# Kernel optimization log

Measured on AMD Instinct MI355X. Metric: run time of the kernel, lower is better.

## Reference

```python
import jax, jax.numpy as jnp
import numpy as np
from jax import lax

B, D, HID, H = 4096, 2048, 2048, 8
HS = HID // H            # head size (also input block size since D == HID)
P = int(HID * 4 / 3)     # 2730 up-projection dim
EPS = 1e-5


def setup_inputs() -> dict:
    key = jax.random.key(0)
    ks = iter(jax.random.split(key, 48))
    def nrm(shape, s=0.02):
        return jax.random.normal(next(ks), shape, jnp.float32) * s
    inp = {
        "x": jax.random.normal(next(ks), (B, D), jnp.float32),
        "h_prev": jax.random.normal(next(ks), (B, HID), jnp.float32),
        "c_prev": jax.random.normal(next(ks), (B, HID), jnp.float32),
        "n_prev": jnp.ones((B, HID), jnp.float32),
        "m_prev": jnp.zeros((B, HID), jnp.float32),
        "ln_w": jnp.ones((D,), jnp.float32),
        "ln_b": jnp.zeros((D,), jnp.float32),
        "conv_w": nrm((1, 1, 4), 0.3),  # Conv1d(1,1,4) kernel
        "conv_b": jnp.zeros((1,), jnp.float32),
        "gn_w": jnp.ones((HID,), jnp.float32),
        "gn_b": jnp.zeros((HID,), jnp.float32),
        "upL_w": nrm((HID, P)), "upL_b": jnp.zeros((P,), jnp.float32),
        "upR_w": nrm((HID, P)), "upR_b": jnp.zeros((P,), jnp.float32),
        "down_w": nrm((P, D)), "down_b": jnp.zeros((D,), jnp.float32),
    }
    # 8 block-diagonal projections: weight [H, block_in, block_out], bias [H, block_out]
    for name in ["Wz", "Wi", "Wf", "Wo", "Rz", "Ri", "Rf", "Ro"]:
        inp[name + "_w"] = nrm((H, HS, HS), 0.05)
        inp[name + "_b"] = jnp.zeros((H, HS), jnp.float32)
    return inp


def _bd(v, w, b):
    # block-diagonal linear: v [B, H*bi], w [H, bi, bo], b [H, bo] -> [B, H*bo]
    Bv = v.shape[0]
    Hn, bi, bo = w.shape
    y = jnp.einsum('bhi,hio->bho', v.reshape(Bv, Hn, bi), w) + b
    return y.reshape(Bv, Hn * bo)


def _forward(x, h_prev, c_prev, n_prev, m_prev, ln_w, ln_b, conv_w, conv_b,
             Wz_w, Wz_b, Wi_w, Wi_b, Wf_w, Wf_b, Wo_w, Wo_b,
             Rz_w, Rz_b, Ri_w, Ri_b, Rf_w, Rf_b, Ro_w, Ro_b,
             gn_w, gn_b, upL_w, upL_b, upR_w, upR_b, down_w, down_b):
    # LayerNorm over features
    mu = x.mean(-1, keepdims=True)
    var = ((x - mu) ** 2).mean(-1, keepdims=True)
    x_norm = (x - mu) * lax.rsqrt(var + EPS) * ln_w + ln_b
    # causal conv1d (kernel 4): left-pad 3, same as padding=3 then crop right 3
    xc = lax.conv_general_dilated(x_norm[:, None, :], conv_w, (1,), [(3, 0)],
                                  dimension_numbers=('NCH', 'OIH', 'NCH'))
    x_conv = jax.nn.silu(xc[:, 0, :] + conv_b)
    # gates via block-diagonal projections
    z = jnp.tanh(_bd(x, Wz_w, Wz_b) + _bd(h_prev, Rz_w, Rz_b))
    o = jax.nn.sigmoid(_bd(x, Wo_w, Wo_b) + _bd(h_prev, Ro_w, Ro_b))
    i_tilde = _bd(x_conv, Wi_w, Wi_b) + _bd(h_prev, Ri_w, Ri_b)
    f_tilde = _bd(x_conv, Wf_w, Wf_b) + _bd(h_prev, Rf_w, Rf_b)
    # stabilized exponential gating
    m_t = jnp.maximum(f_tilde + m_prev, i_tilde)
    i_g = jnp.exp(i_tilde - m_t)
    f_g = jnp.exp(f_tilde + m_prev - m_t)
    c_t = f_g * c_prev + i_g * z
    n_t = f_g * n_prev + i_g
    h_t = o * c_t / n_t
    # GroupNorm(num_heads groups) over hidden
    g = h_t.reshape(-1, H, HS)
    gm = g.mean(-1, keepdims=True)
    gv = ((g - gm) ** 2).mean(-1, keepdims=True)
    gn = ((g - gm) * lax.rsqrt(gv + EPS)).reshape(-1, HID) * gn_w + gn_b
    # gated MLP up/down projection + residual
    left = gn @ upL_w + upL_b
    right = gn @ upR_w + upR_b
    out = (left * jax.nn.gelu(right, approximate=False)) @ down_w + down_b + x
    return out, h_t, c_t, n_t, m_t


def reference(x, h_prev, c_prev, n_prev, m_prev, ln_w, ln_b, conv_w, conv_b,
              Wz_w, Wz_b, Wi_w, Wi_b, Wf_w, Wf_b, Wo_w, Wo_b,
              Rz_w, Rz_b, Ri_w, Ri_b, Rf_w, Rf_b, Ro_w, Ro_b,
              gn_w, gn_b, upL_w, upL_b, upR_w, upR_b, down_w, down_b):
    return _forward(x, h_prev, c_prev, n_prev, m_prev, ln_w, ln_b, conv_w, conv_b,
                    Wz_w, Wz_b, Wi_w, Wi_b, Wf_w, Wf_b, Wo_w, Wo_b,
                    Rz_w, Rz_b, Ri_w, Ri_b, Rf_w, Rf_b, Ro_w, Ro_b,
                    gn_w, gn_b, upL_w, upL_b, upR_w, upR_b, down_w, down_b)
```

## Files before the change

kernel.cpp:

```cpp
#include <hip/hip_runtime.h>
#include <stdint.h>
#include <math.h>

#define Bn   4096
#define Dn   2048
#define Hn   8
#define HSn  256
#define Pn   2730
#define PPADn 2816
#define EPSn 1e-5f

using f32x4  = __attribute__((ext_vector_type(4))) float;
using bf16x8 = __attribute__((ext_vector_type(8))) short;
using u16x4  = __attribute__((ext_vector_type(4))) unsigned short;

__device__ __forceinline__ unsigned short f2bf(float f) {
  union { float f; uint32_t u; } x; x.f = f;
  uint32_t u = x.u;
  return (unsigned short)((u + 0x7FFFu + ((u >> 16) & 1u)) >> 16);
}

__device__ __forceinline__ int xcd_swz(int bid, int n) {
  return (bid & 7) * (n >> 3) + (bid >> 3);
}

#define GLDS(gp, lp) __builtin_amdgcn_global_load_lds(                        \
    (__attribute__((address_space(1))) void*)(size_t)(gp),                    \
    (__attribute__((address_space(3))) void*)(lp), 16, 0, 0)

__device__ __forceinline__ void gemm_mainloop(
    const ushort* __restrict__ A, int lda,
    const ushort* __restrict__ Bt, int ldb,
    int K, int row0, int col0,
    ushort* Asm, ushort* Bsm, f32x4 acc[4][4])
{
  const int tid  = threadIdx.x;
  const int wid  = tid >> 6;
  const int lane = tid & 63;
  const int l16  = lane & 15, lhi = lane >> 4;
  const int wm   = (wid >> 1) * 64, wn = (wid & 1) * 64;
  const int nk   = K >> 6;

  for (int kt = 0; kt < nk; ++kt) {
    __syncthreads();
    #pragma unroll
    for (int q = 0; q < 4; ++q) {
      int ee = q * 256 + tid;
      int r = ee >> 3, c = (ee & 7) << 3;
      const ushort* ga = A  + (size_t)(row0 + r) * lda + (size_t)kt * 64 + c;
      GLDS(ga, (char*)Asm + (q * 4096 + wid * 1024));
      const ushort* gb = Bt + (size_t)(col0 + r) * ldb + (size_t)kt * 64 + c;
      GLDS(gb, (char*)Bsm + (q * 4096 + wid * 1024));
    }
    __syncthreads();
    #pragma unroll
    for (int kk = 0; kk < 2; ++kk) {
      bf16x8 af[4], bfr[4];
      #pragma unroll
      for (int i = 0; i < 4; ++i) {
        af[i]  = *(const bf16x8*)(Asm + (wm + i * 16 + l16) * 64 + kk * 32 + lhi * 8);
        bfr[i] = *(const bf16x8*)(Bsm + (wn + i * 16 + l16) * 64 + kk * 32 + lhi * 8);
      }
      #pragma unroll
      for (int i = 0; i < 4; ++i)
        #pragma unroll
        for (int j = 0; j < 4; ++j)
          acc[i][j] = __builtin_amdgcn_mfma_f32_16x16x32_bf16(af[i], bfr[j], acc[i][j], 0, 0, 0);
    }
  }
}

__global__ void transpose_cvt_kernel(const float* __restrict__ in, ushort* __restrict__ out,
                                     int R, int C, int Rpad, int Cpad)
{
  __shared__ float tile[32][33];
  int r0 = blockIdx.y * 32, c0 = blockIdx.x * 32;
  int tx = threadIdx.x, ty = threadIdx.y;
  #pragma unroll
  for (int i = 0; i < 32; i += 8) {
    int r = r0 + ty + i, c = c0 + tx;
    tile[ty + i][tx] = (r < R && c < C) ? in[(size_t)r * C + c] : 0.f;
  }
  __syncthreads();
  #pragma unroll
  for (int i = 0; i < 32; i += 8) {
    int cc = c0 + ty + i, rr = r0 + tx;
    if (cc < Cpad && rr < Rpad)
      out[(size_t)cc * Rpad + rr] = f2bf(tile[tx][ty + i]);
  }
}

struct Ptr8 { const float* p[8]; };

__global__ void gate_wcvt_kernel(Ptr8 src, ushort* __restrict__ out)
{
  __shared__ float tile[32][33];
  int tz = blockIdx.z;
  int tensor = tz >> 3, h = tz & 7;
  const float* in = src.p[tensor] + (size_t)h * HSn * HSn;
  ushort* o = out + (size_t)tz * HSn * HSn;
  int r0 = blockIdx.y * 32, c0 = blockIdx.x * 32;
  int tx = threadIdx.x, ty = threadIdx.y;
  #pragma unroll
  for (int i = 0; i < 32; i += 8)
    tile[ty + i][tx] = in[(size_t)(r0 + ty + i) * HSn + c0 + tx];
  __syncthreads();
  #pragma unroll
  for (int i = 0; i < 32; i += 8)
    o[(size_t)(c0 + ty + i) * HSn + (r0 + tx)] = f2bf(tile[tx][ty + i]);
}

__global__ void cvt_bf16_kernel(const float* __restrict__ in, ushort* __restrict__ out, int n8)
{
  int idx = blockIdx.x * blockDim.x + threadIdx.x;
  if (idx >= n8) return;
  float4 a = ((const float4*)in)[idx * 2];
  float4 b = ((const float4*)in)[idx * 2 + 1];
  bf16x8 v;
  v[0] = (short)f2bf(a.x); v[1] = (short)f2bf(a.y);
  v[2] = (short)f2bf(a.z); v[3] = (short)f2bf(a.w);
  v[4] = (short)f2bf(b.x); v[5] = (short)f2bf(b.y);
  v[6] = (short)f2bf(b.z); v[7] = (short)f2bf(b.w);
  ((bf16x8*)out)[idx] = v;
}

__global__ __launch_bounds__(256) void ln_conv_kernel(
    const float* __restrict__ x, const float* __restrict__ lnw, const float* __restrict__ lnb,
    const float* __restrict__ convw, const float* __restrict__ convb,
    ushort* __restrict__ xbf, ushort* __restrict__ xcbf)
{
  __shared__ float xn[Dn];
  __shared__ float red[8];
  const int b = blockIdx.x, t = threadIdx.x;
  const float* xr = x + (size_t)b * Dn;
  float4 v0 = ((const float4*)xr)[t * 2];
  float4 v1 = ((const float4*)xr)[t * 2 + 1];
  float xv[8] = {v0.x, v0.y, v0.z, v0.w, v1.x, v1.y, v1.z, v1.w};
  float s = 0.f, s2 = 0.f;
  #pragma unroll
  for (int e = 0; e < 8; ++e) { s += xv[e]; s2 += xv[e] * xv[e]; }
  #pragma unroll
  for (int off = 32; off >= 1; off >>= 1) {
    s  += __shfl_xor(s, off, 64);
    s2 += __shfl_xor(s2, off, 64);
  }
  int wid = t >> 6;
  if ((t & 63) == 0) { red[wid] = s; red[4 + wid] = s2; }
  __syncthreads();
  s  = red[0] + red[1] + red[2] + red[3];
  s2 = red[4] + red[5] + red[6] + red[7];
  float mean = s * (1.f / Dn);
  float var  = s2 * (1.f / Dn) - mean * mean;
  float rstd = rsqrtf(var + EPSn);

  float4 w0 = ((const float4*)lnw)[t * 2], w1 = ((const float4*)lnw)[t * 2 + 1];
  float4 b0 = ((const float4*)lnb)[t * 2], b1 = ((const float4*)lnb)[t * 2 + 1];
  float lw[8] = {w0.x, w0.y, w0.z, w0.w, w1.x, w1.y, w1.z, w1.w};
  float lb[8] = {b0.x, b0.y, b0.z, b0.w, b1.x, b1.y, b1.z, b1.w};
  bf16x8 xb;
  #pragma unroll
  for (int e = 0; e < 8; ++e) {
    int j = t * 8 + e;
    float nv = (xv[e] - mean) * rstd * lw[e] + lb[e];
    xn[j] = nv;
    xb[e] = (short)f2bf(xv[e]);
  }
  ((bf16x8*)(xbf + (size_t)b * Dn))[t] = xb;
  __syncthreads();
  float w[4] = {convw[0], convw[1], convw[2], convw[3]};
  float cb = convb[0];
  bf16x8 cv;
  #pragma unroll
  for (int e = 0; e < 8; ++e) {
    int j = t * 8 + e;
    float a0 = (j >= 3) ? xn[j - 3] : 0.f;
    float a1 = (j >= 2) ? xn[j - 2] : 0.f;
    float a2 = (j >= 1) ? xn[j - 1] : 0.f;
    float v = w[0] * a0 + w[1] * a1 + w[2] * a2 + w[3] * xn[j] + cb;
    float sv = v / (1.f + expf(-v));
    cv[e] = (short)f2bf(sv);
  }
  ((bf16x8*)(xcbf + (size_t)b * Dn))[t] = cv;
}

struct GateArgs { const float* wb[4]; const float* rb[4]; };

__global__ __launch_bounds__(256) void gate_gemm_kernel(
    const ushort* __restrict__ xbf, const ushort* __restrict__ xcbf,
    const ushort* __restrict__ hbf, const ushort* __restrict__ gWt,
    GateArgs gb, float* __restrict__ preact)
{
  __shared__ ushort Asm[128 * 64];
  __shared__ ushort Bsm[128 * 64];
  const int g = blockIdx.z, h = blockIdx.y;
  const int bx = xcd_swz(blockIdx.x, 64);
  const int mt = bx >> 1, nt = bx & 1;
  const int row0 = mt * 128, col0 = nt * 128;
  f32x4 acc[4][4];
  #pragma unroll
  for (int i = 0; i < 4; ++i)
    #pragma unroll
    for (int j = 0; j < 4; ++j) acc[i][j] = f32x4{0.f, 0.f, 0.f, 0.f};

  const ushort* A1 = ((g == 1 || g == 2) ? xcbf : xbf) + h * HSn;
  const ushort* B1 = gWt + (size_t)(g * 8 + h) * (HSn * HSn);
  gemm_mainloop(A1, Dn, B1, HSn, HSn, row0, col0, Asm, Bsm, acc);
  const ushort* A2 = hbf + h * HSn;
  const ushort* B2 = gWt + (size_t)((4 + g) * 8 + h) * (HSn * HSn);
  gemm_mainloop(A2, Dn, B2, HSn, HSn, row0, col0, Asm, Bsm, acc);

  const int tid = threadIdx.x, wid = tid >> 6, lane = tid & 63;
  const int l16 = lane & 15, lhi = lane >> 4;
  const int wm = (wid >> 1) * 64, wn = (wid & 1) * 64;
  float* out = preact + (size_t)g * ((size_t)Bn * Dn);
  const float* wb = gb.wb[g] + h * HSn;
  const float* rb = gb.rb[g] + h * HSn;
  #pragma unroll
  for (int j = 0; j < 4; ++j) {
    int cg = col0 + wn + j * 16 + l16;
    float bias = wb[cg] + rb[cg];
    #pragma unroll
    for (int i = 0; i < 4; ++i) {
      #pragma unroll
      for (int r = 0; r < 4; ++r) {
        int rg = row0 + wm + i * 16 + lhi * 4 + r;
        float v = acc[i][j][r] + bias;
        if (g == 0) v = tanhf(v);
        else if (g == 3) v = 1.f / (1.f + expf(-v));
        out[(size_t)rg * Dn + h * HSn + cg] = v;
      }
    }
  }
}

__global__ __launch_bounds__(64) void gate_pw_gn_kernel(
    const float* __restrict__ preact,
    const float* __restrict__ c_prev, const float* __restrict__ n_prev,
    const float* __restrict__ m_prev,
    const float* __restrict__ gn_w, const float* __restrict__ gn_b,
    float* __restrict__ o_h, float* __restrict__ o_c,
    float* __restrict__ o_n, float* __restrict__ o_m,
    ushort* __restrict__ gnbf)
{
  const int bh = blockIdx.x;
  const int b = bh >> 3, h = bh & 7;
  const int t = threadIdx.x;
  const size_t NE = (size_t)Bn * Dn;
  const size_t base = (size_t)b * Dn + h * HSn + t * 4;

  float4 z4 = *(const float4*)(preact + base);
  float4 i4 = *(const float4*)(preact + NE + base);
  float4 f4 = *(const float4*)(preact + 2 * NE + base);
  float4 o4 = *(const float4*)(preact + 3 * NE + base);
  float4 c4 = *(const float4*)(c_prev + base);
  float4 n4 = *(const float4*)(n_prev + base);
  float4 m4 = *(const float4*)(m_prev + base);

  float za[4] = {z4.x, z4.y, z4.z, z4.w};
  float ia[4] = {i4.x, i4.y, i4.z, i4.w};
  float fa[4] = {f4.x, f4.y, f4.z, f4.w};
  float oa[4] = {o4.x, o4.y, o4.z, o4.w};
  float ca[4] = {c4.x, c4.y, c4.z, c4.w};
  float na[4] = {n4.x, n4.y, n4.z, n4.w};
  float ma[4] = {m4.x, m4.y, m4.z, m4.w};

  float hv[4], mo[4], co[4], no[4];
  float s = 0.f, s2 = 0.f;
  #pragma unroll
  for (int e = 0; e < 4; ++e) {
    float mt = fmaxf(fa[e] + ma[e], ia[e]);
    float ig = expf(ia[e] - mt);
    float fg = expf(fa[e] + ma[e] - mt);
    float ct = fg * ca[e] + ig * za[e];
    float nt = fg * na[e] + ig;
    float ht = oa[e] * ct / nt;
    mo[e] = mt; co[e] = ct; no[e] = nt; hv[e] = ht;
    s += ht; s2 += ht * ht;
  }
  *(float4*)(o_m + base) = make_float4(mo[0], mo[1], mo[2], mo[3]);
  *(float4*)(o_c + base) = make_float4(co[0], co[1], co[2], co[3]);
  *(float4*)(o_n + base) = make_float4(no[0], no[1], no[2], no[3]);
  *(float4*)(o_h + base) = make_float4(hv[0], hv[1], hv[2], hv[3]);

  #pragma unroll
  for (int off = 32; off >= 1; off >>= 1) {
    s  += __shfl_xor(s, off, 64);
    s2 += __shfl_xor(s2, off, 64);
  }
  float mean = s * (1.f / HSn);
  float var  = s2 * (1.f / HSn) - mean * mean;
  float rstd = rsqrtf(var + EPSn);
  u16x4 gv;
  #pragma unroll
  for (int e = 0; e < 4; ++e) {
    int hid = h * HSn + t * 4 + e;
    float gval = (hv[e] - mean) * rstd * gn_w[hid] + gn_b[hid];
    gv[e] = f2bf(gval);
  }
  *(u16x4*)(gnbf + base) = gv;
}

__global__ __launch_bounds__(256) void up_gemm_kernel(
    const ushort* __restrict__ gnbf, const ushort* __restrict__ upt,
    const float* __restrict__ upb, float* __restrict__ leftbuf,
    ushort* __restrict__ actbf, int mode)
{
  __shared__ ushort Asm[128 * 64];
  __shared__ ushort Bsm[128 * 64];
  const int NT = PPADn / 128;
  const int bx = xcd_swz(blockIdx.x, 32 * NT);
  const int mt = bx / NT, nt = bx % NT;
  const int row0 = mt * 128, col0 = nt * 128;
  f32x4 acc[4][4];
  #pragma unroll
  for (int i = 0; i < 4; ++i)
    #pragma unroll
    for (int j = 0; j < 4; ++j) acc[i][j] = f32x4{0.f, 0.f, 0.f, 0.f};

  gemm_mainloop(gnbf, Dn, upt, Dn, Dn, row0, col0, Asm, Bsm, acc);

  const int tid = threadIdx.x, wid = tid >> 6, lane = tid & 63;
  const int l16 = lane & 15, lhi = lane >> 4;
  const int wm = (wid >> 1) * 64, wn = (wid & 1) * 64;
  #pragma unroll
  for (int j = 0; j < 4; ++j) {
    int col = col0 + wn + j * 16 + l16;
    float bias = (col < Pn) ? upb[col] : 0.f;
    #pragma unroll
    for (int i = 0; i < 4; ++i) {
      #pragma unroll
      for (int r = 0; r < 4; ++r) {
        int rg = row0 + wm + i * 16 + lhi * 4 + r;
        float v = acc[i][j][r] + bias;
        size_t idx = (size_t)rg * PPADn + col;
        if (mode == 0) {
          leftbuf[idx] = v;
        } else {
          float ge = 0.5f * v * (1.f + erff(v * 0.70710678118f));
          actbf[idx] = f2bf(leftbuf[idx] * ge);
        }
      }
    }
  }
}

__global__ __launch_bounds__(256) void down_gemm_kernel(
    const ushort* __restrict__ actbf, const ushort* __restrict__ downt,
    const float* __restrict__ downb, const float* __restrict__ x,
    float* __restrict__ outp)
{
  __shared__ ushort Asm[128 * 64];
  __shared__ ushort Bsm[128 * 64];
  const int NT = Dn / 128;
  const int bx = xcd_swz(blockIdx.x, 32 * NT);
  const int mt = bx / NT, nt = bx % NT;
  const int row0 = mt * 128, col0 = nt * 128;
  f32x4 acc[4][4];
  #pragma unroll
  for (int i = 0; i < 4; ++i)
    #pragma unroll
    for (int j = 0; j < 4; ++j) acc[i][j] = f32x4{0.f, 0.f, 0.f, 0.f};

  gemm_mainloop(actbf, PPADn, downt, PPADn, PPADn, row0, col0, Asm, Bsm, acc);

  const int tid = threadIdx.x, wid = tid >> 6, lane = tid & 63;
  const int l16 = lane & 15, lhi = lane >> 4;
  const int wm = (wid >> 1) * 64, wn = (wid & 1) * 64;
  #pragma unroll
  for (int j = 0; j < 4; ++j) {
    int col = col0 + wn + j * 16 + l16;
    float bias = downb[col];
    #pragma unroll
    for (int i = 0; i < 4; ++i) {
      #pragma unroll
      for (int r = 0; r < 4; ++r) {
        int rg = row0 + wm + i * 16 + lhi * 4 + r;
        size_t idx = (size_t)rg * Dn + col;
        outp[idx] = acc[i][j][r] + bias + x[idx];
      }
    }
  }
}

extern "C" void kernel_launch(void* const* d_in, const int* in_sizes, int n_in,
                              void* d_out, int out_size, void* d_ws, size_t ws_size,
                              hipStream_t stream)
{
  const float* x      = (const float*)d_in[0];
  const float* h_prev = (const float*)d_in[1];
  const float* c_prev = (const float*)d_in[2];
  const float* n_prev = (const float*)d_in[3];
  const float* m_prev = (const float*)d_in[4];
  const float* ln_w   = (const float*)d_in[5];
  const float* ln_b   = (const float*)d_in[6];
  const float* conv_w = (const float*)d_in[7];
  const float* conv_b = (const float*)d_in[8];
  const float* gn_w   = (const float*)d_in[9];
  const float* gn_b   = (const float*)d_in[10];
  const float* upL_w  = (const float*)d_in[11];
  const float* upL_b  = (const float*)d_in[12];
  const float* upR_w  = (const float*)d_in[13];
  const float* upR_b  = (const float*)d_in[14];
  const float* down_w = (const float*)d_in[15];
  const float* down_b = (const float*)d_in[16];

  const size_t NE = (size_t)Bn * Dn;

  char* ws = (char*)d_ws;
  size_t off = 0;
  auto alloc = [&](size_t bytes) { void* p = ws + off; off += (bytes + 255) & ~(size_t)255; return p; };
  ushort* xbf   = (ushort*)alloc(NE * 2);
  ushort* xcbf  = (ushort*)alloc(NE * 2);
  ushort* hbf   = (ushort*)alloc(NE * 2);
  ushort* gnbf  = (ushort*)alloc(NE * 2);
  ushort* gWt   = (ushort*)alloc((size_t)8 * Hn * HSn * HSn * 2);
  ushort* upLt  = (ushort*)alloc((size_t)PPADn * Dn * 2);
  ushort* upRt  = (ushort*)alloc((size_t)PPADn * Dn * 2);
  ushort* downt = (ushort*)alloc((size_t)Dn * PPADn * 2);
  float*  preact  = (float*)alloc(4 * NE * 4);
  float*  leftbuf = (float*)preact;
  ushort* actbf   = (ushort*)(preact + (size_t)Bn * PPADn);
  (void)ws_size; (void)in_sizes; (void)n_in; (void)out_size;

  float* out = (float*)d_out;
  float* o_out = out;
  float* o_h = out + NE;
  float* o_c = out + 2 * NE;
  float* o_n = out + 3 * NE;
  float* o_m = out + 4 * NE;

  Ptr8 src;
  src.p[0] = (const float*)d_in[17]; src.p[1] = (const float*)d_in[19];
  src.p[2] = (const float*)d_in[21]; src.p[3] = (const float*)d_in[23];
  src.p[4] = (const float*)d_in[25]; src.p[5] = (const float*)d_in[27];
  src.p[6] = (const float*)d_in[29]; src.p[7] = (const float*)d_in[31];
  gate_wcvt_kernel<<<dim3(8, 8, 64), dim3(32, 8), 0, stream>>>(src, gWt);

  transpose_cvt_kernel<<<dim3(PPADn / 32, Dn / 32), dim3(32, 8), 0, stream>>>(
      upL_w, upLt, Dn, Pn, Dn, PPADn);
  transpose_cvt_kernel<<<dim3(PPADn / 32, Dn / 32), dim3(32, 8), 0, stream>>>(
      upR_w, upRt, Dn, Pn, Dn, PPADn);
  transpose_cvt_kernel<<<dim3(Dn / 32, PPADn / 32), dim3(32, 8), 0, stream>>>(
      down_w, downt, Pn, Dn, PPADn, Dn);

  cvt_bf16_kernel<<<(int)(NE / 8 / 256), 256, 0, stream>>>(h_prev, hbf, (int)(NE / 8));

  ln_conv_kernel<<<Bn, 256, 0, stream>>>(x, ln_w, ln_b, conv_w, conv_b, xbf, xcbf);

  GateArgs ga;
  ga.wb[0] = (const float*)d_in[18]; ga.wb[1] = (const float*)d_in[20];
  ga.wb[2] = (const float*)d_in[22]; ga.wb[3] = (const float*)d_in[24];
  ga.rb[0] = (const float*)d_in[26]; ga.rb[1] = (const float*)d_in[28];
  ga.rb[2] = (const float*)d_in[30]; ga.rb[3] = (const float*)d_in[32];
  gate_gemm_kernel<<<dim3(64, 8, 4), 256, 0, stream>>>(xbf, xcbf, hbf, gWt, ga, preact);

  gate_pw_gn_kernel<<<Bn * Hn, 64, 0, stream>>>(preact, c_prev, n_prev, m_prev,
                                                gn_w, gn_b, o_h, o_c, o_n, o_m, gnbf);

  up_gemm_kernel<<<32 * (PPADn / 128), 256, 0, stream>>>(gnbf, upLt, upL_b, leftbuf, actbf, 0);
  up_gemm_kernel<<<32 * (PPADn / 128), 256, 0, stream>>>(gnbf, upRt, upR_b, leftbuf, actbf, 1);

  down_gemm_kernel<<<32 * (Dn / 128), 256, 0, stream>>>(actbf, downt, down_b, x, o_out);
}
```

Before: 910.4 us.

## Double-buffer LDS tiles in GEMM mainloop to overlap global loads with MFMA

Splits the shared GEMM mainloop into stage and compute helpers and adds a ping-pong LDS buffer pair. The next K-tile is prefetched with global_load_lds while MFMAs run on the current tile, which also drops one barrier per iteration. The gate, up and down GEMM kernels all use the new loop. This doubles LDS per block to 64 KB, which may cut occupancy. The overlap may also be lost if the compiler waits on outstanding vector memory before the LDS reads.

```diff
diff --git a/kernel.cpp b/kernel.cpp
--- a/kernel.cpp
+++ b/kernel.cpp
@@ -28,11 +28,49 @@
     (__attribute__((address_space(1))) void*)(size_t)(gp),                    \
     (__attribute__((address_space(3))) void*)(lp), 16, 0, 0)
 
-__device__ __forceinline__ void gemm_mainloop(
+__device__ __forceinline__ void stage_tile(
+    const ushort* __restrict__ A, int lda,
+    const ushort* __restrict__ Bt, int ldb,
+    int row0, int col0, int kt,
+    ushort* Asm, ushort* Bsm, int tid, int wid)
+{
+  #pragma unroll
+  for (int q = 0; q < 4; ++q) {
+    int ee = q * 256 + tid;
+    int r = ee >> 3, c = (ee & 7) << 3;
+    GLDS(A  + (size_t)(row0 + r) * lda + (size_t)kt * 64 + c,
+         (char*)Asm + (q * 4096 + wid * 1024));
+    GLDS(Bt + (size_t)(col0 + r) * ldb + (size_t)kt * 64 + c,
+         (char*)Bsm + (q * 4096 + wid * 1024));
+  }
+}
+
+__device__ __forceinline__ void compute_tile(
+    const ushort* Asm, const ushort* Bsm, f32x4 acc[4][4],
+    int l16, int lhi, int wm, int wn)
+{
+  #pragma unroll
+  for (int kk = 0; kk < 2; ++kk) {
+    bf16x8 af[4], bfr[4];
+    #pragma unroll
+    for (int i = 0; i < 4; ++i) {
+      af[i]  = *(const bf16x8*)(Asm + (wm + i * 16 + l16) * 64 + kk * 32 + lhi * 8);
+      bfr[i] = *(const bf16x8*)(Bsm + (wn + i * 16 + l16) * 64 + kk * 32 + lhi * 8);
+    }
+    #pragma unroll
+    for (int i = 0; i < 4; ++i)
+      #pragma unroll
+      for (int j = 0; j < 4; ++j)
+        acc[i][j] = __builtin_amdgcn_mfma_f32_16x16x32_bf16(af[i], bfr[j], acc[i][j], 0, 0, 0);
+  }
+}
+
+__device__ __forceinline__ void gemm_mainloop_db(
     const ushort* __restrict__ A, int lda,
     const ushort* __restrict__ Bt, int ldb,
     int K, int row0, int col0,
-    ushort* Asm, ushort* Bsm, f32x4 acc[4][4])
+    ushort* Asm0, ushort* Bsm0, ushort* Asm1, ushort* Bsm1,
+    f32x4 acc[4][4])
 {
   const int tid  = threadIdx.x;
   const int wid  = tid >> 6;
@@ -41,32 +79,16 @@
   const int wm   = (wid >> 1) * 64, wn = (wid & 1) * 64;
   const int nk   = K >> 6;
 
-  for (int kt = 0; kt < nk; ++kt) {
+  stage_tile(A, lda, Bt, ldb, row0, col0, 0, Asm0, Bsm0, tid, wid);
+  __syncthreads();
+  for (int kt = 0; kt < nk; kt += 2) {
+    stage_tile(A, lda, Bt, ldb, row0, col0, kt + 1, Asm1, Bsm1, tid, wid);
+    compute_tile(Asm0, Bsm0, acc, l16, lhi, wm, wn);
     __syncthreads();
-    #pragma unroll
-    for (int q = 0; q < 4; ++q) {
-      int ee = q * 256 + tid;
-      int r = ee >> 3, c = (ee & 7) << 3;
-      const ushort* ga = A  + (size_t)(row0 + r) * lda + (size_t)kt * 64 + c;
-      GLDS(ga, (char*)Asm + (q * 4096 + wid * 1024));
-      const ushort* gb = Bt + (size_t)(col0 + r) * ldb + (size_t)kt * 64 + c;
-      GLDS(gb, (char*)Bsm + (q * 4096 + wid * 1024));
-    }
+    if (kt + 2 < nk)
+      stage_tile(A, lda, Bt, ldb, row0, col0, kt + 2, Asm0, Bsm0, tid, wid);
+    compute_tile(Asm1, Bsm1, acc, l16, lhi, wm, wn);
     __syncthreads();
-    #pragma unroll
-    for (int kk = 0; kk < 2; ++kk) {
-      bf16x8 af[4], bfr[4];
-      #pragma unroll
-      for (int i = 0; i < 4; ++i) {
-        af[i]  = *(const bf16x8*)(Asm + (wm + i * 16 + l16) * 64 + kk * 32 + lhi * 8);
-        bfr[i] = *(const bf16x8*)(Bsm + (wn + i * 16 + l16) * 64 + kk * 32 + lhi * 8);
-      }
-      #pragma unroll
-      for (int i = 0; i < 4; ++i)
-        #pragma unroll
-        for (int j = 0; j < 4; ++j)
-          acc[i][j] = __builtin_amdgcn_mfma_f32_16x16x32_bf16(af[i], bfr[j], acc[i][j], 0, 0, 0);
-    }
   }
 }
 
@@ -190,8 +212,8 @@
     const ushort* __restrict__ hbf, const ushort* __restrict__ gWt,
     GateArgs gb, float* __restrict__ preact)
 {
-  __shared__ ushort Asm[128 * 64];
-  __shared__ ushort Bsm[128 * 64];
+  __shared__ ushort Asm0[128 * 64], Bsm0[128 * 64];
+  __shared__ ushort Asm1[128 * 64], Bsm1[128 * 64];
   const int g = blockIdx.z, h = blockIdx.y;
   const int bx = xcd_swz(blockIdx.x, 64);
   const int mt = bx >> 1, nt = bx & 1;
@@ -204,10 +226,10 @@
 
   const ushort* A1 = ((g == 1 || g == 2) ? xcbf : xbf) + h * HSn;
   const ushort* B1 = gWt + (size_t)(g * 8 + h) * (HSn * HSn);
-  gemm_mainloop(A1, Dn, B1, HSn, HSn, row0, col0, Asm, Bsm, acc);
+  gemm_mainloop_db(A1, Dn, B1, HSn, HSn, row0, col0, Asm0, Bsm0, Asm1, Bsm1, acc);
   const ushort* A2 = hbf + h * HSn;
   const ushort* B2 = gWt + (size_t)((4 + g) * 8 + h) * (HSn * HSn);
-  gemm_mainloop(A2, Dn, B2, HSn, HSn, row0, col0, Asm, Bsm, acc);
+  gemm_mainloop_db(A2, Dn, B2, HSn, HSn, row0, col0, Asm0, Bsm0, Asm1, Bsm1, acc);
 
   const int tid = threadIdx.x, wid = tid >> 6, lane = tid & 63;
   const int l16 = lane & 15, lhi = lane >> 4;
@@ -305,8 +327,8 @@
     const float* __restrict__ upb, float* __restrict__ leftbuf,
     ushort* __restrict__ actbf, int mode)
 {
-  __shared__ ushort Asm[128 * 64];
-  __shared__ ushort Bsm[128 * 64];
+  __shared__ ushort Asm0[128 * 64], Bsm0[128 * 64];
+  __shared__ ushort Asm1[128 * 64], Bsm1[128 * 64];
   const int NT = PPADn / 128;
   const int bx = xcd_swz(blockIdx.x, 32 * NT);
   const int mt = bx / NT, nt = bx % NT;
@@ -317,7 +339,7 @@
     #pragma unroll
     for (int j = 0; j < 4; ++j) acc[i][j] = f32x4{0.f, 0.f, 0.f, 0.f};
 
-  gemm_mainloop(gnbf, Dn, upt, Dn, Dn, row0, col0, Asm, Bsm, acc);
+  gemm_mainloop_db(gnbf, Dn, upt, Dn, Dn, row0, col0, Asm0, Bsm0, Asm1, Bsm1, acc);
 
   const int tid = threadIdx.x, wid = tid >> 6, lane = tid & 63;
   const int l16 = lane & 15, lhi = lane >> 4;
@@ -349,8 +371,8 @@
     const float* __restrict__ downb, const float* __restrict__ x,
     float* __restrict__ outp)
 {
-  __shared__ ushort Asm[128 * 64];
-  __shared__ ushort Bsm[128 * 64];
+  __shared__ ushort Asm0[128 * 64], Bsm0[128 * 64];
+  __shared__ ushort Asm1[128 * 64], Bsm1[128 * 64];
   const int NT = Dn / 128;
   const int bx = xcd_swz(blockIdx.x, 32 * NT);
   const int mt = bx / NT, nt = bx % NT;
@@ -361,7 +383,7 @@
     #pragma unroll
     for (int j = 0; j < 4; ++j) acc[i][j] = f32x4{0.f, 0.f, 0.f, 0.f};
 
-  gemm_mainloop(actbf, PPADn, downt, PPADn, PPADn, row0, col0, Asm, Bsm, acc);
+  gemm_mainloop_db(actbf, PPADn, downt, PPADn, PPADn, row0, col0, Asm0, Bsm0, Asm1, Bsm1, acc);
 
   const int tid = threadIdx.x, wid = tid >> 6, lane = tid & 63;
   const int l16 = lane & 15, lhi = lane >> 4;
```

New measurement: 980.3 us. +7.7%, slower.

## Fuse paired GEMMs sharing the A operand in gate and up projections

Applied to the files above, without the earlier changes.

Adds a dual-B mainloop that loads one A tile and two B tiles per K step and accumulates two outputs, so the shared activation tile is read from memory once. The gate GEMM now computes gate pairs (z,o) and (i,f) per block, halving the grid, and the two up-projection launches are merged into one kernel that applies GELU and the product directly, removing the fp32 left buffer round trip. This doubles the accumulator registers and raises LDS use per block (launch bounds hint 2 blocks), which can cost occupancy or cause spills.

```diff
diff --git a/kernel.cpp b/kernel.cpp
--- a/kernel.cpp
+++ b/kernel.cpp
@@ -47,10 +47,10 @@
     for (int q = 0; q < 4; ++q) {
       int ee = q * 256 + tid;
       int r = ee >> 3, c = (ee & 7) << 3;
-      const ushort* ga = A  + (size_t)(row0 + r) * lda + (size_t)kt * 64 + c;
-      GLDS(ga, (char*)Asm + (q * 4096 + wid * 1024));
-      const ushort* gb = Bt + (size_t)(col0 + r) * ldb + (size_t)kt * 64 + c;
-      GLDS(gb, (char*)Bsm + (q * 4096 + wid * 1024));
+      GLDS(A  + (size_t)(row0 + r) * lda + (size_t)kt * 64 + c,
+           (char*)Asm + (q * 4096 + wid * 1024));
+      GLDS(Bt + (size_t)(col0 + r) * ldb + (size_t)kt * 64 + c,
+           (char*)Bsm + (q * 4096 + wid * 1024));
     }
     __syncthreads();
     #pragma unroll
@@ -66,6 +66,54 @@
         #pragma unroll
         for (int j = 0; j < 4; ++j)
           acc[i][j] = __builtin_amdgcn_mfma_f32_16x16x32_bf16(af[i], bfr[j], acc[i][j], 0, 0, 0);
+    }
+  }
+}
+
+__device__ __forceinline__ void gemm_mainloop2(
+    const ushort* __restrict__ A, int lda,
+    const ushort* __restrict__ B1, const ushort* __restrict__ B2, int ldb,
+    int K, int row0, int col0,
+    ushort* Asm, ushort* B1sm, ushort* B2sm,
+    f32x4 acc1[4][4], f32x4 acc2[4][4])
+{
+  const int tid  = threadIdx.x;
+  const int wid  = tid >> 6;
+  const int lane = tid & 63;
+  const int l16  = lane & 15, lhi = lane >> 4;
+  const int wm   = (wid >> 1) * 64, wn = (wid & 1) * 64;
+  const int nk   = K >> 6;
+
+  for (int kt = 0; kt < nk; ++kt) {
+    __syncthreads();
+    #pragma unroll
+    for (int q = 0; q < 4; ++q) {
+      int ee = q * 256 + tid;
+      int r = ee >> 3, c = (ee & 7) << 3;
+      GLDS(A  + (size_t)(row0 + r) * lda + (size_t)kt * 64 + c,
+           (char*)Asm  + (q * 4096 + wid * 1024));
+      GLDS(B1 + (size_t)(col0 + r) * ldb + (size_t)kt * 64 + c,
+           (char*)B1sm + (q * 4096 + wid * 1024));
+      GLDS(B2 + (size_t)(col0 + r) * ldb + (size_t)kt * 64 + c,
+           (char*)B2sm + (q * 4096 + wid * 1024));
+    }
+    __syncthreads();
+    #pragma unroll
+    for (int kk = 0; kk < 2; ++kk) {
+      bf16x8 af[4], b1f[4], b2f[4];
+      #pragma unroll
+      for (int i = 0; i < 4; ++i) {
+        af[i]  = *(const bf16x8*)(Asm  + (wm + i * 16 + l16) * 64 + kk * 32 + lhi * 8);
+        b1f[i] = *(const bf16x8*)(B1sm + (wn + i * 16 + l16) * 64 + kk * 32 + lhi * 8);
+        b2f[i] = *(const bf16x8*)(B2sm + (wn + i * 16 + l16) * 64 + kk * 32 + lhi * 8);
+      }
+      #pragma unroll
+      for (int i = 0; i < 4; ++i)
+        #pragma unroll
+        for (int j = 0; j < 4; ++j) {
+          acc1[i][j] = __builtin_amdgcn_mfma_f32_16x16x32_bf16(af[i], b1f[j], acc1[i][j], 0, 0, 0);
+          acc2[i][j] = __builtin_amdgcn_mfma_f32_16x16x32_bf16(af[i], b2f[j], acc2[i][j], 0, 0, 0);
+        }
     }
   }
 }
@@ -185,49 +233,59 @@
 
 struct GateArgs { const float* wb[4]; const float* rb[4]; };
 
-__global__ __launch_bounds__(256) void gate_gemm_kernel(
+__global__ __launch_bounds__(256, 2) void gate_gemm_kernel(
     const ushort* __restrict__ xbf, const ushort* __restrict__ xcbf,
     const ushort* __restrict__ hbf, const ushort* __restrict__ gWt,
     GateArgs gb, float* __restrict__ preact)
 {
-  __shared__ ushort Asm[128 * 64];
-  __shared__ ushort Bsm[128 * 64];
-  const int g = blockIdx.z, h = blockIdx.y;
+  __shared__ ushort Asm[128 * 64], B1sm[128 * 64], B2sm[128 * 64];
+  const int p = blockIdx.z, h = blockIdx.y;
+  const int gA = (p == 0) ? 0 : 1;
+  const int gB = (p == 0) ? 3 : 2;
   const int bx = xcd_swz(blockIdx.x, 64);
   const int mt = bx >> 1, nt = bx & 1;
   const int row0 = mt * 128, col0 = nt * 128;
-  f32x4 acc[4][4];
+  f32x4 accA[4][4], accB[4][4];
   #pragma unroll
   for (int i = 0; i < 4; ++i)
     #pragma unroll
-    for (int j = 0; j < 4; ++j) acc[i][j] = f32x4{0.f, 0.f, 0.f, 0.f};
-
-  const ushort* A1 = ((g == 1 || g == 2) ? xcbf : xbf) + h * HSn;
-  const ushort* B1 = gWt + (size_t)(g * 8 + h) * (HSn * HSn);
-  gemm_mainloop(A1, Dn, B1, HSn, HSn, row0, col0, Asm, Bsm, acc);
+    for (int j = 0; j < 4; ++j) { accA[i][j] = f32x4{0.f,0.f,0.f,0.f}; accB[i][j] = f32x4{0.f,0.f,0.f,0.f}; }
+
+  const ushort* A1 = ((p == 0) ? xbf : xcbf) + h * HSn;
+  gemm_mainloop2(A1, Dn,
+                 gWt + (size_t)(gA * 8 + h) * (HSn * HSn),
+                 gWt + (size_t)(gB * 8 + h) * (HSn * HSn), HSn,
+                 HSn, row0, col0, Asm, B1sm, B2sm, accA, accB);
   const ushort* A2 = hbf + h * HSn;
-  const ushort* B2 = gWt + (size_t)((4 + g) * 8 + h) * (HSn * HSn);
-  gemm_mainloop(A2, Dn, B2, HSn, HSn, row0, col0, Asm, Bsm, acc);
+  gemm_mainloop2(A2, Dn,
+                 gWt + (size_t)((4 + gA) * 8 + h) * (HSn * HSn),
+                 gWt + (size_t)((4 + gB) * 8 + h) * (HSn * HSn), HSn,
+                 HSn, row0, col0, Asm, B1sm, B2sm, accA, accB);
 
   const int tid = threadIdx.x, wid = tid >> 6, lane = tid & 63;
   const int l16 = lane & 15, lhi = lane >> 4;
   const int wm = (wid >> 1) * 64, wn = (wid & 1) * 64;
-  float* out = preact + (size_t)g * ((size_t)Bn * Dn);
-  const float* wb = gb.wb[g] + h * HSn;
-  const float* rb = gb.rb[g] + h * HSn;
+  const size_t NE = (size_t)Bn * Dn;
+  float* outA = preact + (size_t)gA * NE;
+  float* outB = preact + (size_t)gB * NE;
+  const float* wbA = gb.wb[gA] + h * HSn;  const float* rbA = gb.rb[gA] + h * HSn;
+  const float* wbB = gb.wb[gB] + h * HSn;  const float* rbB = gb.rb[gB] + h * HSn;
   #pragma unroll
   for (int j = 0; j < 4; ++j) {
     int cg = col0 + wn + j * 16 + l16;
-    float bias = wb[cg] + rb[cg];
+    float biasA = wbA[cg] + rbA[cg];
+    float biasB = wbB[cg] + rbB[cg];
     #pragma unroll
     for (int i = 0; i < 4; ++i) {
       #pragma unroll
       for (int r = 0; r < 4; ++r) {
         int rg = row0 + wm + i * 16 + lhi * 4 + r;
-        float v = acc[i][j][r] + bias;
-        if (g == 0) v = tanhf(v);
-        else if (g == 3) v = 1.f / (1.f + expf(-v));
-        out[(size_t)rg * Dn + h * HSn + cg] = v;
+        float vA = accA[i][j][r] + biasA;
+        float vB = accB[i][j][r] + biasB;
+        if (p == 0) { vA = tanhf(vA); vB = 1.f / (1.f + expf(-vB)); }
+        size_t idx = (size_t)rg * Dn + h * HSn + cg;
+        outA[idx] = vA;
+        outB[idx] = vB;
       }
     }
   }
@@ -300,24 +358,25 @@
   *(u16x4*)(gnbf + base) = gv;
 }
 
-__global__ __launch_bounds__(256) void up_gemm_kernel(
-    const ushort* __restrict__ gnbf, const ushort* __restrict__ upt,
-    const float* __restrict__ upb, float* __restrict__ leftbuf,
-    ushort* __restrict__ actbf, int mode)
-{
-  __shared__ ushort Asm[128 * 64];
-  __shared__ ushort Bsm[128 * 64];
+__global__ __launch_bounds__(256, 2) void up_fused_kernel(
+    const ushort* __restrict__ gnbf,
+    const ushort* __restrict__ upLt, const ushort* __restrict__ upRt,
+    const float* __restrict__ upLb, const float* __restrict__ upRb,
+    ushort* __restrict__ actbf)
+{
+  __shared__ ushort Asm[128 * 64], B1sm[128 * 64], B2sm[128 * 64];
   const int NT = PPADn / 128;
   const int bx = xcd_swz(blockIdx.x, 32 * NT);
   const int mt = bx / NT, nt = bx % NT;
   const int row0 = mt * 128, col0 = nt * 128;
-  f32x4 acc[4][4];
+  f32x4 accL[4][4], accR[4][4];
   #pragma unroll
   for (int i = 0; i < 4; ++i)
     #pragma unroll
-    for (int j = 0; j < 4; ++j) acc[i][j] = f32x4{0.f, 0.f, 0.f, 0.f};
-
-  gemm_mainloop(gnbf, Dn, upt, Dn, Dn, row0, col0, Asm, Bsm, acc);
+    for (int j = 0; j < 4; ++j) { accL[i][j] = f32x4{0.f,0.f,0.f,0.f}; accR[i][j] = f32x4{0.f,0.f,0.f,0.f}; }
+
+  gemm_mainloop2(gnbf, Dn, upLt, upRt, Dn, Dn, row0, col0,
+                 Asm, B1sm, B2sm, accL, accR);
 
   const int tid = threadIdx.x, wid = tid >> 6, lane = tid & 63;
   const int l16 = lane & 15, lhi = lane >> 4;
@@ -325,20 +384,17 @@
   #pragma unroll
   for (int j = 0; j < 4; ++j) {
     int col = col0 + wn + j * 16 + l16;
-    float bias = (col < Pn) ? upb[col] : 0.f;
+    float bL = (col < Pn) ? upLb[col] : 0.f;
+    float bR = (col < Pn) ? upRb[col] : 0.f;
     #pragma unroll
     for (int i = 0; i < 4; ++i) {
       #pragma unroll
       for (int r = 0; r < 4; ++r) {
         int rg = row0 + wm + i * 16 + lhi * 4 + r;
-        float v = acc[i][j][r] + bias;
-        size_t idx = (size_t)rg * PPADn + col;
-        if (mode == 0) {
-          leftbuf[idx] = v;
-        } else {
-          float ge = 0.5f * v * (1.f + erff(v * 0.70710678118f));
-          actbf[idx] = f2bf(leftbuf[idx] * ge);
-        }
+        float lv = accL[i][j][r] + bL;
+        float rv = accR[i][j][r] + bR;
+        float ge = 0.5f * rv * (1.f + erff(rv * 0.70710678118f));
+        actbf[(size_t)rg * PPADn + col] = f2bf(lv * ge);
       }
     }
   }
@@ -397,11 +453,8 @@
   const float* conv_b = (const float*)d_in[8];
   const float* gn_w   = (const float*)d_in[9];
   const float* gn_b   = (const float*)d_in[10];
-  const float* upL_w  = (const float*)d_in[11];
   const float* upL_b  = (const float*)d_in[12];
-  const float* upR_w  = (const float*)d_in[13];
   const float* upR_b  = (const float*)d_in[14];
-  const float* down_w = (const float*)d_in[15];
   const float* down_b = (const float*)d_in[16];
 
   const size_t NE = (size_t)Bn * Dn;
@@ -418,8 +471,7 @@
   ushort* upRt  = (ushort*)alloc((size_t)PPADn * Dn * 2);
   ushort* downt = (ushort*)alloc((size_t)Dn * PPADn * 2);
   float*  preact  = (float*)alloc(4 * NE * 4);
-  float*  leftbuf = (float*)preact;
-  ushort* actbf   = (ushort*)(preact + (size_t)Bn * PPADn);
+  ushort* actbf   = (ushort*)preact;
   (void)ws_size; (void)in_sizes; (void)n_in; (void)out_size;
 
   float* out = (float*)d_out;
@@ -437,11 +489,11 @@
   gate_wcvt_kernel<<<dim3(8, 8, 64), dim3(32, 8), 0, stream>>>(src, gWt);
 
   transpose_cvt_kernel<<<dim3(PPADn / 32, Dn / 32), dim3(32, 8), 0, stream>>>(
-      upL_w, upLt, Dn, Pn, Dn, PPADn);
+      (const float*)d_in[11], upLt, Dn, Pn, Dn, PPADn);
   transpose_cvt_kernel<<<dim3(PPADn / 32, Dn / 32), dim3(32, 8), 0, stream>>>(
-      upR_w, upRt, Dn, Pn, Dn, PPADn);
+      (const float*)d_in[13], upRt, Dn, Pn, Dn, PPADn);
   transpose_cvt_kernel<<<dim3(Dn / 32, PPADn / 32), dim3(32, 8), 0, stream>>>(
-      down_w, downt, Pn, Dn, PPADn, Dn);
+      (const float*)d_in[15], downt, Pn, Dn, PPADn, Dn);
 
   cvt_bf16_kernel<<<(int)(NE / 8 / 256), 256, 0, stream>>>(h_prev, hbf, (int)(NE / 8));
 
@@ -452,13 +504,13 @@
   ga.wb[2] = (const float*)d_in[22]; ga.wb[3] = (const float*)d_in[24];
   ga.rb[0] = (const float*)d_in[26]; ga.rb[1] = (const float*)d_in[28];
   ga.rb[2] = (const float*)d_in[30]; ga.rb[3] = (const float*)d_in[32];
-  gate_gemm_kernel<<<dim3(64, 8, 4), 256, 0, stream>>>(xbf, xcbf, hbf, gWt, ga, preact);
+  gate_gemm_kernel<<<dim3(64, 8, 2), 256, 0, stream>>>(xbf, xcbf, hbf, gWt, ga, preact);
 
   gate_pw_gn_kernel<<<Bn * Hn, 64, 0, stream>>>(preact, c_prev, n_prev, m_prev,
                                                 gn_w, gn_b, o_h, o_c, o_n, o_m, gnbf);
 
-  up_gemm_kernel<<<32 * (PPADn / 128), 256, 0, stream>>>(gnbf, upLt, upL_b, leftbuf, actbf, 0);
-  up_gemm_kernel<<<32 * (PPADn / 128), 256, 0, stream>>>(gnbf, upRt, upR_b, leftbuf, actbf, 1);
+  up_fused_kernel<<<32 * (PPADn / 128), 256, 0, stream>>>(gnbf, upLt, upRt,
+                                                          upL_b, upR_b, actbf);
 
   down_gemm_kernel<<<32 * (Dn / 128), 256, 0, stream>>>(actbf, downt, down_b, x, o_out);
 }
```

Measured after the change: 813.8 us. -10.6%, faster.
